# Optimization experiments

Hardware: AMD Instinct MI355X
Metric: run time of the kernel (lower is better)

The kernel has to match this reference:

```python
import jax, jax.numpy as jnp
import numpy as np

B, C, H, W = 8, 256, 32, 32
N, COND_DIM, KV_DIM, REL_DIM = 512, 512, 512, 64
N_HEADS = 8
D_HEAD = KV_DIM // N_HEADS
K_SEL = int(N * 0.6)  # auto mode, shallow layer (layer_idx=2 < total_layers//2=4) -> centrality, ratio_shallow=0.6
NEG = -1e9


def _linear_params(key, fan_in, fan_out):
    kw, kb = jax.random.split(key)
    w = jax.random.normal(kw, (fan_out, fan_in), dtype=jnp.float32) / np.sqrt(fan_in)
    b = jax.random.normal(kb, (fan_out,), dtype=jnp.float32) * 0.01
    return w, b


def _normalize(x, axis=-1):
    # torch F.normalize: x / max(||x||_2, eps)
    n = jnp.sqrt(jnp.sum(x * x, axis=axis, keepdims=True))
    return x / jnp.maximum(n, 1e-12)


def setup_inputs() -> dict:
    key = jax.random.key(0)
    ks = jax.random.split(key, 10)
    h = jax.random.normal(ks[0], (B, C, H, W), dtype=jnp.float32)
    cond_feats = jax.random.normal(ks[1], (B, N, COND_DIM), dtype=jnp.float32)
    cond_mask = jax.random.randint(ks[2], (B, N), 0, 2) > 0  # bool, 1 valid
    Wq, bq = _linear_params(ks[3], C, KV_DIM)
    Wk, bk = _linear_params(ks[4], COND_DIM, KV_DIM)
    Wv, bv = _linear_params(ks[5], COND_DIM, KV_DIM)
    Wrq, brq = _linear_params(ks[6], C, REL_DIM)
    Wrk, brk = _linear_params(ks[7], COND_DIM, REL_DIM)
    Wo, bo = _linear_params(ks[8], KV_DIM, C)
    return dict(h=h, cond_feats=cond_feats, cond_mask=cond_mask,
                Wq=Wq, bq=bq, Wk=Wk, bk=bk, Wv=Wv, bv=bv,
                Wrq=Wrq, brq=brq, Wrk=Wrk, brk=brk, Wo=Wo, bo=bo)


def reference(h, cond_feats, cond_mask, Wq, bq, Wk, bk, Wv, bv, Wrq, brq, Wrk, brk, Wo, bo):
    Bq, Ch, Hh, Ww = h.shape
    S = Hh * Ww
    # ---- q/k/v projections ----
    q = h.reshape(Bq, Ch, S).transpose(0, 2, 1)                # (B,S,C)
    q = q @ Wq.T + bq                                           # (B,S,KV)
    K = cond_feats @ Wk.T + bk                                  # (B,N,KV)
    V = cond_feats @ Wv.T + bv
    qh = q.reshape(Bq, S, N_HEADS, D_HEAD).transpose(0, 2, 1, 3)
    kh = K.reshape(Bq, N, N_HEADS, D_HEAD).transpose(0, 2, 1, 3)
    vh = V.reshape(Bq, N, N_HEADS, D_HEAD).transpose(0, 2, 1, 3)
    attn_scores = jnp.einsum('bhqd,bhkd->bhqk', qh, kh) / np.sqrt(D_HEAD)
    # ---- selector: auto mode, shallow -> centrality scores ----
    qg = h.mean(axis=(2, 3))                                    # adaptive_avg_pool2d(h,1) -> (B,C)
    qg_proj = _normalize(qg @ Wrq.T + brq)                      # (B,REL)  (unused branch kept faithful)
    cond_proj = _normalize(cond_feats @ Wrk.T + brk)            # (B,N,REL)
    Smat = jnp.einsum('bnd,bmd->bnm', cond_proj, cond_proj)     # (B,N,N)
    eye = jnp.eye(N, dtype=bool)
    centrality = jnp.where(eye[None], 0.0, Smat).sum(axis=-1)   # (B,N)
    scores = centrality
    # ---- top-k mask via scatter ----
    topk_idx = jax.lax.top_k(scores, K_SEL)[1]                  # (B,K)
    selected = jnp.zeros((Bq, N), dtype=bool).at[jnp.arange(Bq)[:, None], topk_idx].set(True)
    allowed = selected & cond_mask
    rows_all_false = ~allowed.any(axis=1)                       # (B,)
    idx0 = jnp.argmax(scores, axis=-1)                          # top-1 fallback
    fallback = jax.nn.one_hot(idx0, N, dtype=bool)
    allowed = allowed | (rows_all_false[:, None] & fallback)
    attn_scores = jnp.where(allowed[:, None, None, :], attn_scores, NEG)
    # ---- attention ----
    attn = jax.nn.softmax(attn_scores, axis=-1)
    out = jnp.einsum('bhqk,bhkd->bhqd', attn, vh)               # (B,h,S,d)
    out = out.transpose(0, 2, 1, 3).reshape(Bq, S, KV_DIM)
    out = out @ Wo.T + bo                                       # (B,S,C)
    return out.transpose(0, 2, 1).reshape(Bq, Ch, Hh, Ww)
```

## Files before the change

kernel.cpp:

```cpp
#include <hip/hip_runtime.h>
#include <math.h>

#define B_ 8
#define C_ 256
#define S_ 1024
#define N_ 512
#define KV_ 512
#define REL_ 64
#define NH_ 8
#define DH_ 64
#define KSEL_ 307

typedef __attribute__((ext_vector_type(8))) short bf16x8;
typedef __attribute__((ext_vector_type(4))) short short4v;
typedef __attribute__((ext_vector_type(4))) float f32x4;

__device__ __forceinline__ short f2bf(float f) {
  unsigned int u = __float_as_uint(f);
  u += 0x7fffu + ((u >> 16) & 1u);
  return (short)(u >> 16);
}

__global__ __launch_bounds__(256) void k_prep(const float* __restrict__ cond, const float* __restrict__ Wq,
                                              const float* __restrict__ Wk, const float* __restrict__ Wv,
                                              const float* __restrict__ Wo, const float* __restrict__ h,
                                              const float* __restrict__ Wrk,
                                              short* __restrict__ cond_b, short* __restrict__ Wq_b,
                                              short* __restrict__ Wk_b, short* __restrict__ Wv_b,
                                              short* __restrict__ Wo_b, short* __restrict__ hT,
                                              float* __restrict__ cp_part) {
  __shared__ float fs[2176];
  int blk = blockIdx.x, tid = threadIdx.x;
  if (blk < 2816) {
    const float* src; short* dst; int base;
    if (blk < 2048)      { src = cond; dst = cond_b; base = blk; }
    else if (blk < 2176) { src = Wq;   dst = Wq_b;   base = blk - 2048; }
    else if (blk < 2432) { src = Wk;   dst = Wk_b;   base = blk - 2176; }
    else if (blk < 2688) { src = Wv;   dst = Wv_b;   base = blk - 2432; }
    else                 { src = Wo;   dst = Wo_b;   base = blk - 2688; }
    int i = base * 256 + tid;
    float4 v = ((const float4*)src)[i];
    short4v o = { f2bf(v.x), f2bf(v.y), f2bf(v.z), f2bf(v.w) };
    ((short4v*)dst)[i] = o;
  } else if (blk < 4864) {
    int i = blk - 2816;
    int s0 = (i & 31) * 32, c0 = ((i >> 5) & 7) * 32, b = i >> 8;
    int x = tid & 31, y0 = tid >> 5;
    #pragma unroll
    for (int y = y0; y < 32; y += 8)
      fs[y * 33 + x] = h[((size_t)(b * C_ + c0 + y)) * S_ + s0 + x];
    __syncthreads();
    #pragma unroll
    for (int y = y0; y < 32; y += 8)
      hT[((size_t)(b * S_ + s0 + y)) * C_ + c0 + x] = f2bf(fs[x * 33 + y]);
  } else {
    int i = blk - 4864;
    int bm = (i & 63) * 64, kb = i >> 6;
    float* As = fs;
    float* Bs = fs + 1088;
    int tm = (tid >> 4) << 2, tn = (tid & 15) << 2;
    float acc[4][4] = {};
    for (int k0 = kb * 64; k0 < kb * 64 + 64; k0 += 16) {
      #pragma unroll
      for (int ii = 0; ii < 4; ++ii) {
        int idx = tid + ii * 256;
        int r = idx >> 4, k = idx & 15;
        As[r * 17 + k] = cond[(size_t)(bm + r) * KV_ + k0 + k];
        Bs[r * 17 + k] = Wrk[(size_t)r * KV_ + k0 + k];
      }
      __syncthreads();
      #pragma unroll
      for (int k = 0; k < 16; ++k) {
        float a[4], bb[4];
        #pragma unroll
        for (int x = 0; x < 4; ++x) { a[x] = As[(tm + x) * 17 + k]; bb[x] = Bs[(tn + x) * 17 + k]; }
        #pragma unroll
        for (int x = 0; x < 4; ++x)
          #pragma unroll
          for (int y = 0; y < 4; ++y)
            acc[x][y] += a[x] * bb[y];
      }
      __syncthreads();
    }
    #pragma unroll
    for (int x = 0; x < 4; ++x)
      #pragma unroll
      for (int y = 0; y < 4; ++y)
        cp_part[(size_t)kb * 262144 + (size_t)(bm + tm + x) * 64 + tn + y] = acc[x][y];
  }
}

__global__ __launch_bounds__(256) void k_normalize(const float* __restrict__ cp_part, const float* __restrict__ brk,
                                                   float* __restrict__ cp) {
  int row = blockIdx.x * 4 + (threadIdx.x >> 6);
  int d = threadIdx.x & 63;
  size_t off = (size_t)row * 64 + d;
  float x = brk[d];
  #pragma unroll
  for (int s = 0; s < 8; ++s) x += cp_part[(size_t)s * 262144 + off];
  float ss = x * x;
  #pragma unroll
  for (int o = 32; o; o >>= 1) ss += __shfl_xor(ss, o);
  cp[off] = x / fmaxf(sqrtf(ss), 1e-12f);
}

__global__ __launch_bounds__(512) void k_select(const float* __restrict__ cp, const int* __restrict__ mask,
                                                int* __restrict__ idxb, int* __restrict__ cnt) {
  int b = blockIdx.x, tid = threadIdx.x;
  __shared__ float part[8][64];
  __shared__ float vsum[64];
  __shared__ float sc[512];
  __shared__ int wcnt[8];
  int d = tid & 63, g = tid >> 6;
  float sacc = 0.f;
  for (int n = g * 64; n < g * 64 + 64; ++n)
    sacc += cp[((size_t)b * N_ + n) * 64 + d];
  part[g][d] = sacc;
  __syncthreads();
  if (tid < 64) {
    float v = 0.f;
    #pragma unroll
    for (int gg = 0; gg < 8; ++gg) v += part[gg][tid];
    vsum[tid] = v;
  }
  __syncthreads();
  const float* x = cp + ((size_t)b * N_ + tid) * 64;
  float dsum = 0.f, dself = 0.f;
  #pragma unroll
  for (int dd = 0; dd < 64; ++dd) {
    float xv = x[dd];
    dsum += xv * vsum[dd];
    dself += xv * xv;
  }
  sc[tid] = dsum - dself;
  __syncthreads();
  float v = sc[tid];
  int rank = 0;
  for (int j = 0; j < N_; ++j) {
    float u = sc[j];
    rank += (u > v) || (u == v && j < tid);
  }
  int sel = (rank < KSEL_) && (mask[b * N_ + tid] != 0);
  unsigned long long bal = __ballot(sel);
  if ((tid & 63) == 0) wcnt[g] = __popcll(bal);
  __syncthreads();
  int off2 = 0, total = 0;
  #pragma unroll
  for (int i = 0; i < 8; ++i) { int c = wcnt[i]; total += c; if (i < g) off2 += c; }
  int pos = off2 + __popcll(bal & ((1ull << (tid & 63)) - 1ull));
  if (sel) idxb[b * N_ + pos] = tid;
  if (total == 0 && rank == 0) idxb[b * N_] = tid;
  if (tid == 0) cnt[b] = (total == 0) ? 1 : total;
}

template<int MODE, int GA, int GB, int WM>
__device__ __forceinline__ void gemm_body(const short* __restrict__ A, const short* __restrict__ W,
                                          const float* __restrict__ bias, void* __restrict__ Cout,
                                          short* As, short* Bs, size_t bm, size_t bn, int Kd, int Nout,
                                          const int* __restrict__ gidx, int cntv) {
  constexpr int BMv = WM * 32;
  constexpr int NIA = BMv / 64;
  constexpr int OPS = NIA + 2;
  int tid = threadIdx.x;
  int lane = tid & 63, wid = tid >> 6;
  int wr = wid >> 1, wc = wid & 1;
  f32x4 acc[WM][4] = {};
  int srow = lane >> 2;
  int schunk = lane & 3;
  int steps = Kd >> 5;

  int rowA[NIA ? NIA : 1], rowB[2];
  #pragma unroll
  for (int i = 0; i < NIA; ++i) {
    int rt = wid * (WM * 8) + i * 16 + srow;
    rowA[i] = GA ? (((int)bm + rt < cntv) ? gidx[bm + rt] : 0) : (int)(bm + rt);
  }
  #pragma unroll
  for (int i = 0; i < 2; ++i) {
    int rt = wid * 32 + i * 16 + srow;
    rowB[i] = GB ? (((int)bn + rt < cntv) ? gidx[bn + rt] : 0) : (int)(bn + rt);
  }

  #define STAGE_G(t, buf)                                                                              \
    {                                                                                                  \
      int k0s = (t) * 32;                                                                              \
      _Pragma("unroll")                                                                                \
      for (int i = 0; i < NIA; ++i) {                                                                  \
        int rt = wid * (WM * 8) + i * 16 + srow;                                                       \
        int sc_ = (schunk ^ ((rt >> 1) & 3)) * 8;                                                      \
        const short* ga = A + (size_t)rowA[i] * Kd + k0s + sc_;                                        \
        __builtin_amdgcn_global_load_lds((const __attribute__((address_space(1))) void*)ga,            \
            (__attribute__((address_space(3))) void*)(As + (buf) * (BMv * 32) +                        \
                                                     (wid * (WM * 8) + i * 16) * 32),                  \
            16, 0, 0);                                                                                 \
      }                                                                                                \
      _Pragma("unroll")                                                                                \
      for (int i = 0; i < 2; ++i) {                                                                    \
        int rt = wid * 32 + i * 16 + srow;                                                             \
        int sc_ = (schunk ^ ((rt >> 1) & 3)) * 8;                                                      \
        const short* gb = W + (size_t)rowB[i] * Kd + k0s + sc_;                                        \
        __builtin_amdgcn_global_load_lds((const __attribute__((address_space(1))) void*)gb,            \
            (__attribute__((address_space(3))) void*)(Bs + (buf) * 4096 + (wid * 32 + i * 16) * 32),   \
            16, 0, 0);                                                                                 \
      }                                                                                                \
    }

  STAGE_G(0, 0);
  STAGE_G(1, 1);

  int cur = 0;
  for (int t = 0; t < steps; ++t) {
    if (t == steps - 1)
      asm volatile("s_waitcnt vmcnt(0)" ::: "memory");
    else
      asm volatile("s_waitcnt vmcnt(%0)" :: "n"(OPS) : "memory");
    __syncthreads();
    if (t + 2 < steps) {
      int nb = cur + 2; if (nb >= 3) nb -= 3;
      STAGE_G(t + 2, nb);
    }
    const short* Ac = As + cur * (BMv * 32);
    const short* Bc = Bs + cur * 4096;
    bf16x8 a[WM], b[4];
    #pragma unroll
    for (int m = 0; m < WM; ++m) {
      int rt = wr * (WM * 16) + m * 16 + (lane & 15);
      a[m] = *(const bf16x8*)(Ac + rt * 32 + (((lane >> 4) ^ ((rt >> 1) & 3)) * 8));
    }
    #pragma unroll
    for (int n = 0; n < 4; ++n) {
      int rt = wc * 64 + n * 16 + (lane & 15);
      b[n] = *(const bf16x8*)(Bc + rt * 32 + (((lane >> 4) ^ ((rt >> 1) & 3)) * 8));
    }
    __builtin_amdgcn_s_setprio(1);
    #pragma unroll
    for (int m = 0; m < WM; ++m)
      #pragma unroll
      for (int n = 0; n < 4; ++n)
        acc[m][n] = __builtin_amdgcn_mfma_f32_16x16x32_bf16(a[m], b[n], acc[m][n], 0, 0, 0);
    __builtin_amdgcn_s_setprio(0);
    cur = (cur == 2) ? 0 : cur + 1;
  }
  #undef STAGE_G

  int c0 = lane & 15, r0q = lane >> 4;
  #pragma unroll
  for (int n = 0; n < 4; ++n) {
    size_t col = bn + wc * 64 + n * 16 + c0;
    #pragma unroll
    for (int m = 0; m < WM; ++m) {
      #pragma unroll
      for (int j = 0; j < 4; ++j) {
        size_t row = bm + wr * (WM * 16) + m * 16 + r0q * 4 + j;
        if (MODE == 0) {
          ((short*)Cout)[row * Nout + col] = f2bf(acc[m][n][j] + bias[col]);
        } else if (MODE == 1) {
          ((float*)Cout)[((col >> 10) * C_ + row) * S_ + (col & (S_ - 1))] = acc[m][n][j] + bias[row];
        } else {
          ((short*)Cout)[row * Nout + col] = f2bf(acc[m][n][j] + bias[row]);
        }
      }
    }
  }
}

__global__ __launch_bounds__(256) void k_fused_proj(const short* __restrict__ hT, const short* __restrict__ cond_b,
                                                    const short* __restrict__ Wq_b, const short* __restrict__ Wk_b,
                                                    const short* __restrict__ Wv_b,
                                                    const float* __restrict__ bq, const float* __restrict__ bk,
                                                    const float* __restrict__ bv,
                                                    short* __restrict__ qb, short* __restrict__ Kc,
                                                    short* __restrict__ Vtc,
                                                    const int* __restrict__ idxb, const int* __restrict__ cnt) {
  __shared__ short smem[24576];
  int blk = blockIdx.x;
  if (blk < 96) {
    int b = blk / 12, j = blk % 12;
    int mt = j >> 2, ntile = j & 3;
    int cv = cnt[b], padded = (cv + 63) & ~63;
    if (mt * 128 >= padded) return;
    gemm_body<0, 1, 0, 4>(cond_b + (size_t)b * N_ * KV_, Wk_b, bk, Kc + (size_t)b * N_ * KV_,
                          smem, smem + 12288, (size_t)mt * 128, (size_t)ntile * 128, KV_, KV_,
                          idxb + b * N_, cv);
  } else if (blk < 192) {
    int i = blk - 96, b = i / 12, j = i % 12;
    int mtd = j & 3, ntc = j >> 2;
    int cv = cnt[b], padded = (cv + 63) & ~63;
    if (ntc * 128 >= padded) return;
    gemm_body<3, 0, 1, 4>(Wv_b, cond_b + (size_t)b * N_ * KV_, bv, Vtc + (size_t)b * 512 * N_,
                          smem, smem + 12288, (size_t)mtd * 128, (size_t)ntc * 128, KV_, N_,
                          idxb + b * N_, cv);
  } else {
    int i = blk - 192;
    gemm_body<0, 0, 0, 4>(hT, Wq_b, bq, qb, smem, smem + 12288,
                          (size_t)(i & 63) * 128, (size_t)(i >> 6) * 128, C_, KV_, nullptr, 0);
  }
}

__device__ __forceinline__ void stage_tile64(const short* gRowBase, int gStride, short* ldsBase, int wid, int lane) {
  int sub = lane >> 3;
  int colE = ((lane & 7) ^ sub) * 8;
  #pragma unroll
  for (int i = 0; i < 2; ++i) {
    int r = wid * 16 + i * 8 + sub;
    const short* gp = gRowBase + (size_t)r * gStride + colE;
    __builtin_amdgcn_global_load_lds((const __attribute__((address_space(1))) void*)gp,
                                     (__attribute__((address_space(3))) void*)(ldsBase + wid * 1024 + i * 512),
                                     16, 0, 0);
  }
}
__device__ __forceinline__ void stage_tile64_w8(const short* gRowBase, int gStride, short* ldsBase, int wid, int lane) {
  int sub = lane >> 3;
  int colE = ((lane & 7) ^ sub) * 8;
  int r = wid * 8 + sub;
  const short* gp = gRowBase + (size_t)r * gStride + colE;
  __builtin_amdgcn_global_load_lds((const __attribute__((address_space(1))) void*)gp,
                                   (__attribute__((address_space(3))) void*)(ldsBase + wid * 512),
                                   16, 0, 0);
}

#define QK2L 0.18033688f
__global__ __launch_bounds__(512) void k_attn_mfma(const short* __restrict__ qb, const short* __restrict__ Kc,
                                                   const short* __restrict__ Vtc, const int* __restrict__ cnt,
                                                   short* __restrict__ attn_b) {
  __shared__ short Qs[8192];
  __shared__ short Ks[2][4096];
  __shared__ short Vs[2][4096];
  short* Ps = Qs;
  int g = blockIdx.x;
  int xcd = g & 7, li = g >> 3;
  int bh = xcd * 8 + (li >> 3);
  int qt = li & 7;
  int b = bh >> 3, h = bh & 7;
  int tid = threadIdx.x, lane = tid & 63, wid = tid >> 6;
  int hi = lane >> 4, q = lane & 15;
  int s0 = qt * 128;
  int cntv = cnt[b];
  int nt = (cntv + 63) >> 6;
  const short* Qg = qb + ((size_t)(b * S_ + s0) * KV_ + h * DH_);
  const short* Kg = Kc + ((size_t)(b * N_) * KV_ + h * DH_);
  const short* Vg = Vtc + ((size_t)((b * NH_ + h) * DH_) * N_);

  stage_tile64(Qg, KV_, Qs, wid, lane);
  stage_tile64_w8(Kg, KV_, Ks[0], wid, lane);
  stage_tile64_w8(Vg, N_, Vs[0], wid, lane);
  asm volatile("s_waitcnt vmcnt(0)" ::: "memory");
  __syncthreads();

  int swz = (lane & 7) << 3;
  bf16x8 qf0 = *(const bf16x8*)&Qs[(wid * 16 + q) * 64 + ((hi * 8) ^ swz)];
  bf16x8 qf1 = *(const bf16x8*)&Qs[(wid * 16 + q) * 64 + ((32 + hi * 8) ^ swz)];

  float m = -1e30f, l = 0.f;
  f32x4 o[4] = {};

  for (int t = 0; t < nt; ++t) {
    int cur = t & 1;
    const short* Kcur = Ks[cur];
    const short* Vcur = Vs[cur];
    if (t + 1 < nt) {
      stage_tile64_w8(Kg + (size_t)(t + 1) * 64 * KV_, KV_, Ks[cur ^ 1], wid, lane);
      stage_tile64_w8(Vg + (t + 1) * 64, N_, Vs[cur ^ 1], wid, lane);
    }
    f32x4 pv[4];
    __builtin_amdgcn_s_setprio(1);
    #pragma unroll
    for (int kf = 0; kf < 4; ++kf) {
      bf16x8 k0 = *(const bf16x8*)&Kcur[(kf * 16 + q) * 64 + ((hi * 8) ^ swz)];
      bf16x8 k1 = *(const bf16x8*)&Kcur[(kf * 16 + q) * 64 + ((32 + hi * 8) ^ swz)];
      f32x4 z = {0.f, 0.f, 0.f, 0.f};
      pv[kf] = __builtin_amdgcn_mfma_f32_16x16x32_bf16(k0, qf0, z, 0, 0, 0);
      pv[kf] = __builtin_amdgcn_mfma_f32_16x16x32_bf16(k1, qf1, pv[kf], 0, 0, 0);
    }
    __builtin_amdgcn_s_setprio(0);
    float sv[16];
    int kbase = t * 64 + hi * 4;
    #pragma unroll
    for (int kf = 0; kf < 4; ++kf) {
      #pragma unroll
      for (int r = 0; r < 4; ++r)
        sv[kf * 4 + r] = (kbase + kf * 16 + r < cntv) ? pv[kf][r] * QK2L : -1e30f;
    }
    float tmax = sv[0];
    #pragma unroll
    for (int i = 1; i < 16; ++i) tmax = fmaxf(tmax, sv[i]);
    tmax = fmaxf(tmax, __shfl_xor(tmax, 16));
    tmax = fmaxf(tmax, __shfl_xor(tmax, 32));
    float mnew = fmaxf(m, tmax);
    float scale = exp2f(m - mnew);
    float psum = 0.f;
    #pragma unroll
    for (int i = 0; i < 16; ++i) { sv[i] = exp2f(sv[i] - mnew); psum += sv[i]; }
    psum += __shfl_xor(psum, 16);
    psum += __shfl_xor(psum, 32);
    l = l * scale + psum;
    m = mnew;
    #pragma unroll
    for (int df = 0; df < 4; ++df) {
      o[df][0] *= scale; o[df][1] *= scale; o[df][2] *= scale; o[df][3] *= scale;
    }
    int pbase = wid * 1024 + q * 64;
    #pragma unroll
    for (int kf = 0; kf < 4; ++kf) {
      short4v pk = { f2bf(sv[kf * 4 + 0]), f2bf(sv[kf * 4 + 1]), f2bf(sv[kf * 4 + 2]), f2bf(sv[kf * 4 + 3]) };
      *(short4v*)&Ps[pbase + ((kf * 16 + hi * 4) ^ swz)] = pk;
    }
    __builtin_amdgcn_s_setprio(1);
    #pragma unroll
    for (int ks = 0; ks < 2; ++ks) {
      bf16x8 pb = *(const bf16x8*)&Ps[pbase + ((ks * 32 + hi * 8) ^ swz)];
      #pragma unroll
      for (int df = 0; df < 4; ++df) {
        bf16x8 vf = *(const bf16x8*)&Vcur[(df * 16 + q) * 64 + ((ks * 32 + hi * 8) ^ swz)];
        o[df] = __builtin_amdgcn_mfma_f32_16x16x32_bf16(vf, pb, o[df], 0, 0, 0);
      }
    }
    __builtin_amdgcn_s_setprio(0);
    asm volatile("s_waitcnt vmcnt(0)" ::: "memory");
    __syncthreads();
  }
  float inv = 1.0f / l;
  short* op = attn_b + ((size_t)(b * S_ + s0 + wid * 16 + q) * KV_ + h * DH_);
  #pragma unroll
  for (int df = 0; df < 4; ++df) {
    short4v ov = { f2bf(o[df][0] * inv), f2bf(o[df][1] * inv), f2bf(o[df][2] * inv), f2bf(o[df][3] * inv) };
    *(short4v*)&op[df * 16 + hi * 4] = ov;
  }
}

__global__ __launch_bounds__(256) void k_outproj(const short* __restrict__ Wo_b, const short* __restrict__ attn_b,
                                                 const float* __restrict__ bo, float* __restrict__ out) {
  __shared__ short smem[18432];
  gemm_body<1, 0, 0, 2>(Wo_b, attn_b, bo, out, smem, smem + 6144,
                        (size_t)blockIdx.x * 64, (size_t)blockIdx.y * 128, KV_, B_ * S_, nullptr, 0);
}

extern "C" void kernel_launch(void* const* d_in, const int* in_sizes, int n_in,
                              void* d_out, int out_size, void* d_ws, size_t ws_size,
                              hipStream_t stream) {
  const float* h         = (const float*)d_in[0];
  const float* cond      = (const float*)d_in[1];
  const int*   cond_mask = (const int*)d_in[2];
  const float* Wq = (const float*)d_in[3];
  const float* bq = (const float*)d_in[4];
  const float* Wk = (const float*)d_in[5];
  const float* bk = (const float*)d_in[6];
  const float* Wv = (const float*)d_in[7];
  const float* bv = (const float*)d_in[8];
  const float* Wrk = (const float*)d_in[11];
  const float* brk = (const float*)d_in[12];
  const float* Wo  = (const float*)d_in[13];
  const float* bo  = (const float*)d_in[14];
  float* out = (float*)d_out;

  char* w = (char*)d_ws;
  short* qb      = (short*)(w + 0);
  short* Kc      = (short*)(w + 8388608);
  short* Vtc     = (short*)(w + 12582912);
  short* attn_b  = (short*)(w + 16777216);
  short* hT      = (short*)(w + 25165824);
  short* cond_b  = (short*)(w + 29360128);
  float* cp_part = (float*)(w + 33554432);
  float* cp      = (float*)(w + 41943040);
  int*   idxb    = (int*)  (w + 42991616);
  int*   cnt     = (int*)  (w + 43008000);
  short* Wq_b    = (short*)(w + 43008064);
  short* Wk_b    = (short*)(w + 43270208);
  short* Wv_b    = (short*)(w + 43794496);
  short* Wo_b    = (short*)(w + 44318784);

  k_prep<<<5376, 256, 0, stream>>>(cond, Wq, Wk, Wv, Wo, h, Wrk,
                                   cond_b, Wq_b, Wk_b, Wv_b, Wo_b, hT, cp_part);
  k_normalize<<<1024, 256, 0, stream>>>(cp_part, brk, cp);
  k_select<<<8, 512, 0, stream>>>(cp, cond_mask, idxb, cnt);
  k_fused_proj<<<448, 256, 0, stream>>>(hT, cond_b, Wq_b, Wk_b, Wv_b, bq, bk, bv,
                                        qb, Kc, Vtc, idxb, cnt);
  k_attn_mfma<<<512, 512, 0, stream>>>(qb, Kc, Vtc, cnt, attn_b);
  k_outproj<<<dim3(4, 64), 256, 0, stream>>>(Wo_b, attn_b, bo, out);
}
```

Baseline: 98.95 us.

## Fuse post-prep kernels into one persistent megakernel with grid barriers

```diff
diff --git a/kernel.cpp b/kernel.cpp
--- a/kernel.cpp
+++ b/kernel.cpp
@@ -10,6 +10,7 @@
 #define NH_ 8
 #define DH_ 64
 #define KSEL_ 307
+#define NBLK_ 512
 
 typedef __attribute__((ext_vector_type(8))) short bf16x8;
 typedef __attribute__((ext_vector_type(4))) short short4v;
@@ -19,6 +20,16 @@
   unsigned int u = __float_as_uint(f);
   u += 0x7fffu + ((u >> 16) & 1u);
   return (short)(u >> 16);
+}
+
+__device__ __forceinline__ void grid_barrier(int* bar, int target) {
+  __syncthreads();
+  if (threadIdx.x == 0) {
+    __hip_atomic_fetch_add(bar, 1, __ATOMIC_RELEASE, __HIP_MEMORY_SCOPE_AGENT);
+    while (__hip_atomic_load(bar, __ATOMIC_ACQUIRE, __HIP_MEMORY_SCOPE_AGENT) < target)
+      __builtin_amdgcn_s_sleep(2);
+  }
+  __syncthreads();
 }
 
 __global__ __launch_bounds__(256) void k_prep(const float* __restrict__ cond, const float* __restrict__ Wq,
@@ -90,69 +101,6 @@
   }
 }
 
-__global__ __launch_bounds__(256) void k_normalize(const float* __restrict__ cp_part, const float* __restrict__ brk,
-                                                   float* __restrict__ cp) {
-  int row = blockIdx.x * 4 + (threadIdx.x >> 6);
-  int d = threadIdx.x & 63;
-  size_t off = (size_t)row * 64 + d;
-  float x = brk[d];
-  #pragma unroll
-  for (int s = 0; s < 8; ++s) x += cp_part[(size_t)s * 262144 + off];
-  float ss = x * x;
-  #pragma unroll
-  for (int o = 32; o; o >>= 1) ss += __shfl_xor(ss, o);
-  cp[off] = x / fmaxf(sqrtf(ss), 1e-12f);
-}
-
-__global__ __launch_bounds__(512) void k_select(const float* __restrict__ cp, const int* __restrict__ mask,
-                                                int* __restrict__ idxb, int* __restrict__ cnt) {
-  int b = blockIdx.x, tid = threadIdx.x;
-  __shared__ float part[8][64];
-  __shared__ float vsum[64];
-  __shared__ float sc[512];
-  __shared__ int wcnt[8];
-  int d = tid & 63, g = tid >> 6;
-  float sacc = 0.f;
-  for (int n = g * 64; n < g * 64 + 64; ++n)
-    sacc += cp[((size_t)b * N_ + n) * 64 + d];
-  part[g][d] = sacc;
-  __syncthreads();
-  if (tid < 64) {
-    float v = 0.f;
-    #pragma unroll
-    for (int gg = 0; gg < 8; ++gg) v += part[gg][tid];
-    vsum[tid] = v;
-  }
-  __syncthreads();
-  const float* x = cp + ((size_t)b * N_ + tid) * 64;
-  float dsum = 0.f, dself = 0.f;
-  #pragma unroll
-  for (int dd = 0; dd < 64; ++dd) {
-    float xv = x[dd];
-    dsum += xv * vsum[dd];
-    dself += xv * xv;
-  }
-  sc[tid] = dsum - dself;
-  __syncthreads();
-  float v = sc[tid];
-  int rank = 0;
-  for (int j = 0; j < N_; ++j) {
-    float u = sc[j];
-    rank += (u > v) || (u == v && j < tid);
-  }
-  int sel = (rank < KSEL_) && (mask[b * N_ + tid] != 0);
-  unsigned long long bal = __ballot(sel);
-  if ((tid & 63) == 0) wcnt[g] = __popcll(bal);
-  __syncthreads();
-  int off2 = 0, total = 0;
-  #pragma unroll
-  for (int i = 0; i < 8; ++i) { int c = wcnt[i]; total += c; if (i < g) off2 += c; }
-  int pos = off2 + __popcll(bal & ((1ull << (tid & 63)) - 1ull));
-  if (sel) idxb[b * N_ + pos] = tid;
-  if (total == 0 && rank == 0) idxb[b * N_] = tid;
-  if (tid == 0) cnt[b] = (total == 0) ? 1 : total;
-}
-
 template<int MODE, int GA, int GB, int WM>
 __device__ __forceinline__ void gemm_body(const short* __restrict__ A, const short* __restrict__ W,
                                           const float* __restrict__ bias, void* __restrict__ Cout,
@@ -264,39 +212,6 @@
   }
 }
 
-__global__ __launch_bounds__(256) void k_fused_proj(const short* __restrict__ hT, const short* __restrict__ cond_b,
-                                                    const short* __restrict__ Wq_b, const short* __restrict__ Wk_b,
-                                                    const short* __restrict__ Wv_b,
-                                                    const float* __restrict__ bq, const float* __restrict__ bk,
-                                                    const float* __restrict__ bv,
-                                                    short* __restrict__ qb, short* __restrict__ Kc,
-                                                    short* __restrict__ Vtc,
-                                                    const int* __restrict__ idxb, const int* __restrict__ cnt) {
-  __shared__ short smem[24576];
-  int blk = blockIdx.x;
-  if (blk < 96) {
-    int b = blk / 12, j = blk % 12;
-    int mt = j >> 2, ntile = j & 3;
-    int cv = cnt[b], padded = (cv + 63) & ~63;
-    if (mt * 128 >= padded) return;
-    gemm_body<0, 1, 0, 4>(cond_b + (size_t)b * N_ * KV_, Wk_b, bk, Kc + (size_t)b * N_ * KV_,
-                          smem, smem + 12288, (size_t)mt * 128, (size_t)ntile * 128, KV_, KV_,
-                          idxb + b * N_, cv);
-  } else if (blk < 192) {
-    int i = blk - 96, b = i / 12, j = i % 12;
-    int mtd = j & 3, ntc = j >> 2;
-    int cv = cnt[b], padded = (cv + 63) & ~63;
-    if (ntc * 128 >= padded) return;
-    gemm_body<3, 0, 1, 4>(Wv_b, cond_b + (size_t)b * N_ * KV_, bv, Vtc + (size_t)b * 512 * N_,
-                          smem, smem + 12288, (size_t)mtd * 128, (size_t)ntc * 128, KV_, N_,
-                          idxb + b * N_, cv);
-  } else {
-    int i = blk - 192;
-    gemm_body<0, 0, 0, 4>(hT, Wq_b, bq, qb, smem, smem + 12288,
-                          (size_t)(i & 63) * 128, (size_t)(i >> 6) * 128, C_, KV_, nullptr, 0);
-  }
-}
-
 __device__ __forceinline__ void stage_tile64(const short* gRowBase, int gStride, short* ldsBase, int wid, int lane) {
   int sub = lane >> 3;
   int colE = ((lane & 7) ^ sub) * 8;
@@ -309,130 +224,241 @@
                                      16, 0, 0);
   }
 }
-__device__ __forceinline__ void stage_tile64_w8(const short* gRowBase, int gStride, short* ldsBase, int wid, int lane) {
-  int sub = lane >> 3;
-  int colE = ((lane & 7) ^ sub) * 8;
-  int r = wid * 8 + sub;
-  const short* gp = gRowBase + (size_t)r * gStride + colE;
-  __builtin_amdgcn_global_load_lds((const __attribute__((address_space(1))) void*)gp,
-                                   (__attribute__((address_space(3))) void*)(ldsBase + wid * 512),
-                                   16, 0, 0);
-}
 
 #define QK2L 0.18033688f
-__global__ __launch_bounds__(512) void k_attn_mfma(const short* __restrict__ qb, const short* __restrict__ Kc,
-                                                   const short* __restrict__ Vtc, const int* __restrict__ cnt,
-                                                   short* __restrict__ attn_b) {
-  __shared__ short Qs[8192];
-  __shared__ short Ks[2][4096];
-  __shared__ short Vs[2][4096];
-  short* Ps = Qs;
-  int g = blockIdx.x;
-  int xcd = g & 7, li = g >> 3;
-  int bh = xcd * 8 + (li >> 3);
-  int qt = li & 7;
-  int b = bh >> 3, h = bh & 7;
-  int tid = threadIdx.x, lane = tid & 63, wid = tid >> 6;
-  int hi = lane >> 4, q = lane & 15;
-  int s0 = qt * 128;
-  int cntv = cnt[b];
-  int nt = (cntv + 63) >> 6;
-  const short* Qg = qb + ((size_t)(b * S_ + s0) * KV_ + h * DH_);
-  const short* Kg = Kc + ((size_t)(b * N_) * KV_ + h * DH_);
-  const short* Vg = Vtc + ((size_t)((b * NH_ + h) * DH_) * N_);
-
-  stage_tile64(Qg, KV_, Qs, wid, lane);
-  stage_tile64_w8(Kg, KV_, Ks[0], wid, lane);
-  stage_tile64_w8(Vg, N_, Vs[0], wid, lane);
-  asm volatile("s_waitcnt vmcnt(0)" ::: "memory");
-  __syncthreads();
-
-  int swz = (lane & 7) << 3;
-  bf16x8 qf0 = *(const bf16x8*)&Qs[(wid * 16 + q) * 64 + ((hi * 8) ^ swz)];
-  bf16x8 qf1 = *(const bf16x8*)&Qs[(wid * 16 + q) * 64 + ((32 + hi * 8) ^ swz)];
-
-  float m = -1e30f, l = 0.f;
-  f32x4 o[4] = {};
-
-  for (int t = 0; t < nt; ++t) {
-    int cur = t & 1;
-    const short* Kcur = Ks[cur];
-    const short* Vcur = Vs[cur];
-    if (t + 1 < nt) {
-      stage_tile64_w8(Kg + (size_t)(t + 1) * 64 * KV_, KV_, Ks[cur ^ 1], wid, lane);
-      stage_tile64_w8(Vg + (t + 1) * 64, N_, Vs[cur ^ 1], wid, lane);
-    }
-    f32x4 pv[4];
-    __builtin_amdgcn_s_setprio(1);
-    #pragma unroll
-    for (int kf = 0; kf < 4; ++kf) {
-      bf16x8 k0 = *(const bf16x8*)&Kcur[(kf * 16 + q) * 64 + ((hi * 8) ^ swz)];
-      bf16x8 k1 = *(const bf16x8*)&Kcur[(kf * 16 + q) * 64 + ((32 + hi * 8) ^ swz)];
-      f32x4 z = {0.f, 0.f, 0.f, 0.f};
-      pv[kf] = __builtin_amdgcn_mfma_f32_16x16x32_bf16(k0, qf0, z, 0, 0, 0);
-      pv[kf] = __builtin_amdgcn_mfma_f32_16x16x32_bf16(k1, qf1, pv[kf], 0, 0, 0);
-    }
-    __builtin_amdgcn_s_setprio(0);
-    float sv[16];
-    int kbase = t * 64 + hi * 4;
-    #pragma unroll
-    for (int kf = 0; kf < 4; ++kf) {
-      #pragma unroll
-      for (int r = 0; r < 4; ++r)
-        sv[kf * 4 + r] = (kbase + kf * 16 + r < cntv) ? pv[kf][r] * QK2L : -1e30f;
-    }
-    float tmax = sv[0];
-    #pragma unroll
-    for (int i = 1; i < 16; ++i) tmax = fmaxf(tmax, sv[i]);
-    tmax = fmaxf(tmax, __shfl_xor(tmax, 16));
-    tmax = fmaxf(tmax, __shfl_xor(tmax, 32));
-    float mnew = fmaxf(m, tmax);
-    float scale = exp2f(m - mnew);
-    float psum = 0.f;
-    #pragma unroll
-    for (int i = 0; i < 16; ++i) { sv[i] = exp2f(sv[i] - mnew); psum += sv[i]; }
-    psum += __shfl_xor(psum, 16);
-    psum += __shfl_xor(psum, 32);
-    l = l * scale + psum;
-    m = mnew;
-    #pragma unroll
-    for (int df = 0; df < 4; ++df) {
-      o[df][0] *= scale; o[df][1] *= scale; o[df][2] *= scale; o[df][3] *= scale;
-    }
-    int pbase = wid * 1024 + q * 64;
-    #pragma unroll
-    for (int kf = 0; kf < 4; ++kf) {
-      short4v pk = { f2bf(sv[kf * 4 + 0]), f2bf(sv[kf * 4 + 1]), f2bf(sv[kf * 4 + 2]), f2bf(sv[kf * 4 + 3]) };
-      *(short4v*)&Ps[pbase + ((kf * 16 + hi * 4) ^ swz)] = pk;
-    }
-    __builtin_amdgcn_s_setprio(1);
-    #pragma unroll
-    for (int ks = 0; ks < 2; ++ks) {
-      bf16x8 pb = *(const bf16x8*)&Ps[pbase + ((ks * 32 + hi * 8) ^ swz)];
+__global__ __launch_bounds__(256, 2) void k_mega(
+    const float* __restrict__ cp_part, const float* __restrict__ brk, float* __restrict__ cp,
+    const int* __restrict__ cond_mask, int* __restrict__ idxb, int* __restrict__ cnt,
+    const short* __restrict__ hT, const short* __restrict__ cond_b,
+    const short* __restrict__ Wq_b, const short* __restrict__ Wk_b, const short* __restrict__ Wv_b,
+    const float* __restrict__ bq, const float* __restrict__ bk, const float* __restrict__ bv,
+    short* __restrict__ qb, short* __restrict__ Kc, short* __restrict__ Vtc,
+    short* __restrict__ attn_b, const short* __restrict__ Wo_b, const float* __restrict__ bo,
+    float* __restrict__ out, int* __restrict__ bar) {
+  __shared__ char smem_raw[49152];
+  int bid = blockIdx.x, tid = threadIdx.x;
+
+  {
+    int wid = tid >> 6, d = tid & 63;
+    #pragma unroll
+    for (int i = 0; i < 2; ++i) {
+      int row = (bid * 4 + wid) * 2 + i;
+      size_t off = (size_t)row * 64 + d;
+      float x = brk[d];
+      #pragma unroll
+      for (int s = 0; s < 8; ++s) x += cp_part[(size_t)s * 262144 + off];
+      float ss = x * x;
+      #pragma unroll
+      for (int o = 32; o; o >>= 1) ss += __shfl_xor(ss, o);
+      cp[off] = x / fmaxf(sqrtf(ss), 1e-12f);
+    }
+  }
+  grid_barrier(bar, NBLK_);
+
+  if (bid < 8) {
+    float* part = (float*)smem_raw;
+    float* vsum = part + 256;
+    float* sc   = vsum + 64;
+    int*   wcnt = (int*)(sc + 512);
+    int b = bid;
+    int d = tid & 63, g = tid >> 6;
+    float sacc = 0.f;
+    for (int n = g * 128; n < g * 128 + 128; ++n)
+      sacc += cp[((size_t)b * N_ + n) * 64 + d];
+    part[g * 64 + d] = sacc;
+    __syncthreads();
+    if (tid < 64) vsum[tid] = part[tid] + part[64 + tid] + part[128 + tid] + part[192 + tid];
+    __syncthreads();
+    #pragma unroll
+    for (int rr = 0; rr < 2; ++rr) {
+      int n = tid + rr * 256;
+      const float* x = cp + ((size_t)b * N_ + n) * 64;
+      float dsum = 0.f, dself = 0.f;
+      #pragma unroll
+      for (int dd = 0; dd < 64; ++dd) {
+        float xv = x[dd];
+        dsum += xv * vsum[dd];
+        dself += xv * xv;
+      }
+      sc[n] = dsum - dself;
+    }
+    __syncthreads();
+    int sel[2], rank[2];
+    #pragma unroll
+    for (int rr = 0; rr < 2; ++rr) {
+      int n = tid + rr * 256;
+      float v = sc[n];
+      int r = 0;
+      for (int j = 0; j < N_; ++j) {
+        float u = sc[j];
+        r += (u > v) || (u == v && j < n);
+      }
+      rank[rr] = r;
+      sel[rr] = (r < KSEL_) && (cond_mask[b * N_ + n] != 0);
+    }
+    unsigned long long bal0 = __ballot(sel[0]);
+    unsigned long long bal1 = __ballot(sel[1]);
+    if ((tid & 63) == 0) { wcnt[g] = __popcll(bal0); wcnt[4 + g] = __popcll(bal1); }
+    __syncthreads();
+    int off0 = 0, off4 = 0, total = 0;
+    #pragma unroll
+    for (int c = 0; c < 8; ++c) {
+      int cc = wcnt[c];
+      total += cc;
+      if (c < g) off0 += cc;
+      if (c < 4 + g) off4 += cc;
+    }
+    unsigned long long lmask = (1ull << (tid & 63)) - 1ull;
+    if (sel[0]) idxb[b * N_ + off0 + __popcll(bal0 & lmask)] = tid;
+    if (sel[1]) idxb[b * N_ + off4 + __popcll(bal1 & lmask)] = tid + 256;
+    if (total == 0) {
+      if (rank[0] == 0) idxb[b * N_] = tid;
+      if (rank[1] == 0) idxb[b * N_] = tid + 256;
+    }
+    if (tid == 0) cnt[b] = (total == 0) ? 1 : total;
+  }
+  grid_barrier(bar, 2 * NBLK_);
+
+  {
+    short* As = (short*)smem_raw;
+    short* Bs = As + 12288;
+    if (bid < 96) {
+      int b = bid / 12, j = bid % 12;
+      int mt = j >> 2, ntile = j & 3;
+      int cv = cnt[b], padded = (cv + 63) & ~63;
+      if (mt * 128 < padded)
+        gemm_body<0, 1, 0, 4>(cond_b + (size_t)b * N_ * KV_, Wk_b, bk, Kc + (size_t)b * N_ * KV_,
+                              As, Bs, (size_t)mt * 128, (size_t)ntile * 128, KV_, KV_,
+                              idxb + b * N_, cv);
+    } else if (bid < 192) {
+      int i = bid - 96, b = i / 12, j = i % 12;
+      int mtd = j & 3, ntc = j >> 2;
+      int cv = cnt[b], padded = (cv + 63) & ~63;
+      if (ntc * 128 < padded)
+        gemm_body<3, 0, 1, 4>(Wv_b, cond_b + (size_t)b * N_ * KV_, bv, Vtc + (size_t)b * 512 * N_,
+                              As, Bs, (size_t)mtd * 128, (size_t)ntc * 128, KV_, N_,
+                              idxb + b * N_, cv);
+    } else if (bid < 448) {
+      int i = bid - 192;
+      gemm_body<0, 0, 0, 4>(hT, Wq_b, bq, qb, As, Bs,
+                            (size_t)(i & 63) * 128, (size_t)(i >> 6) * 128, C_, KV_, nullptr, 0);
+    }
+  }
+  grid_barrier(bar, 3 * NBLK_);
+
+  {
+    short* Qs  = (short*)smem_raw;
+    short* KsB = Qs + 4096;
+    short* VsB = KsB + 8192;
+    short* Ps  = Qs;
+    int lane = tid & 63, wid = tid >> 6;
+    int hi = lane >> 4, q = lane & 15;
+    int swz = (lane & 7) << 3;
+    for (int it = 0; it < 2; ++it) {
+      int job = bid * 2 + it;
+      int bh = job >> 4, qt = job & 15;
+      int b = bh >> 3, h = bh & 7;
+      int s0 = qt * 64;
+      int cntv = cnt[b];
+      int nt = (cntv + 63) >> 6;
+      const short* Qg = qb + ((size_t)(b * S_ + s0) * KV_ + h * DH_);
+      const short* Kg = Kc + ((size_t)(b * N_) * KV_ + h * DH_);
+      const short* Vg = Vtc + ((size_t)b * 512 + h * DH_) * N_;
+
+      stage_tile64(Qg, KV_, Qs, wid, lane);
+      stage_tile64(Kg, KV_, KsB, wid, lane);
+      stage_tile64(Vg, N_, VsB, wid, lane);
+      asm volatile("s_waitcnt vmcnt(0)" ::: "memory");
+      __syncthreads();
+
+      bf16x8 qf0 = *(const bf16x8*)&Qs[(wid * 16 + q) * 64 + ((hi * 8) ^ swz)];
+      bf16x8 qf1 = *(const bf16x8*)&Qs[(wid * 16 + q) * 64 + ((32 + hi * 8) ^ swz)];
+
+      float m = -1e30f, l = 0.f;
+      f32x4 o[4] = {};
+
+      for (int t = 0; t < nt; ++t) {
+        int cur = t & 1;
+        const short* Kcur = KsB + cur * 4096;
+        const short* Vcur = VsB + cur * 4096;
+        if (t + 1 < nt) {
+          stage_tile64(Kg + (size_t)(t + 1) * 64 * KV_, KV_, KsB + (cur ^ 1) * 4096, wid, lane);
+          stage_tile64(Vg + (t + 1) * 64, N_, VsB + (cur ^ 1) * 4096, wid, lane);
+        }
+        f32x4 pv[4];
+        __builtin_amdgcn_s_setprio(1);
+        #pragma unroll
+        for (int kf = 0; kf < 4; ++kf) {
+          bf16x8 k0 = *(const bf16x8*)&Kcur[(kf * 16 + q) * 64 + ((hi * 8) ^ swz)];
+          bf16x8 k1 = *(const bf16x8*)&Kcur[(kf * 16 + q) * 64 + ((32 + hi * 8) ^ swz)];
+          f32x4 z = {0.f, 0.f, 0.f, 0.f};
+          pv[kf] = __builtin_amdgcn_mfma_f32_16x16x32_bf16(k0, qf0, z, 0, 0, 0);
+          pv[kf] = __builtin_amdgcn_mfma_f32_16x16x32_bf16(k1, qf1, pv[kf], 0, 0, 0);
+        }
+        __builtin_amdgcn_s_setprio(0);
+        float sv[16];
+        int kbase = t * 64 + hi * 4;
+        #pragma unroll
+        for (int kf = 0; kf < 4; ++kf) {
+          #pragma unroll
+          for (int r = 0; r < 4; ++r)
+            sv[kf * 4 + r] = (kbase + kf * 16 + r < cntv) ? pv[kf][r] * QK2L : -1e30f;
+        }
+        float tmax = sv[0];
+        #pragma unroll
+        for (int i = 1; i < 16; ++i) tmax = fmaxf(tmax, sv[i]);
+        tmax = fmaxf(tmax, __shfl_xor(tmax, 16));
+        tmax = fmaxf(tmax, __shfl_xor(tmax, 32));
+        float mnew = fmaxf(m, tmax);
+        float scale = exp2f(m - mnew);
+        float psum = 0.f;
+        #pragma unroll
+        for (int i = 0; i < 16; ++i) { sv[i] = exp2f(sv[i] - mnew); psum += sv[i]; }
+        psum += __shfl_xor(psum, 16);
+        psum += __shfl_xor(psum, 32);
+        l = l * scale + psum;
+        m = mnew;
+        #pragma unroll
+        for (int df = 0; df < 4; ++df) {
+          o[df][0] *= scale; o[df][1] *= scale; o[df][2] *= scale; o[df][3] *= scale;
+        }
+        int pbase = wid * 1024 + q * 64;
+        #pragma unroll
+        for (int kf = 0; kf < 4; ++kf) {
+          short4v pk = { f2bf(sv[kf * 4 + 0]), f2bf(sv[kf * 4 + 1]), f2bf(sv[kf * 4 + 2]), f2bf(sv[kf * 4 + 3]) };
+          *(short4v*)&Ps[pbase + ((kf * 16 + hi * 4) ^ swz)] = pk;
+        }
+        __builtin_amdgcn_s_setprio(1);
+        #pragma unroll
+        for (int ks = 0; ks < 2; ++ks) {
+          bf16x8 pb = *(const bf16x8*)&Ps[pbase + ((ks * 32 + hi * 8) ^ swz)];
+          #pragma unroll
+          for (int df = 0; df < 4; ++df) {
+            bf16x8 vf = *(const bf16x8*)&Vcur[(df * 16 + q) * 64 + ((ks * 32 + hi * 8) ^ swz)];
+            o[df] = __builtin_amdgcn_mfma_f32_16x16x32_bf16(vf, pb, o[df], 0, 0, 0);
+          }
+        }
+        __builtin_amdgcn_s_setprio(0);
+        asm volatile("s_waitcnt vmcnt(0)" ::: "memory");
+        __syncthreads();
+      }
+      float inv = 1.0f / l;
+      short* op = attn_b + ((size_t)(b * S_ + s0 + wid * 16 + q) * KV_ + h * DH_);
       #pragma unroll
       for (int df = 0; df < 4; ++df) {
-        bf16x8 vf = *(const bf16x8*)&Vcur[(df * 16 + q) * 64 + ((ks * 32 + hi * 8) ^ swz)];
-        o[df] = __builtin_amdgcn_mfma_f32_16x16x32_bf16(vf, pb, o[df], 0, 0, 0);
-      }
-    }
-    __builtin_amdgcn_s_setprio(0);
-    asm volatile("s_waitcnt vmcnt(0)" ::: "memory");
-    __syncthreads();
-  }
-  float inv = 1.0f / l;
-  short* op = attn_b + ((size_t)(b * S_ + s0 + wid * 16 + q) * KV_ + h * DH_);
-  #pragma unroll
-  for (int df = 0; df < 4; ++df) {
-    short4v ov = { f2bf(o[df][0] * inv), f2bf(o[df][1] * inv), f2bf(o[df][2] * inv), f2bf(o[df][3] * inv) };
-    *(short4v*)&op[df * 16 + hi * 4] = ov;
-  }
-}
-
-__global__ __launch_bounds__(256) void k_outproj(const short* __restrict__ Wo_b, const short* __restrict__ attn_b,
-                                                 const float* __restrict__ bo, float* __restrict__ out) {
-  __shared__ short smem[18432];
-  gemm_body<1, 0, 0, 2>(Wo_b, attn_b, bo, out, smem, smem + 6144,
-                        (size_t)blockIdx.x * 64, (size_t)blockIdx.y * 128, KV_, B_ * S_, nullptr, 0);
+        short4v ov = { f2bf(o[df][0] * inv), f2bf(o[df][1] * inv), f2bf(o[df][2] * inv), f2bf(o[df][3] * inv) };
+        *(short4v*)&op[df * 16 + hi * 4] = ov;
+      }
+    }
+  }
+  grid_barrier(bar, 4 * NBLK_);
+
+  if (bid < 256) {
+    short* As = (short*)smem_raw;
+    short* Bs = As + 6144;
+    gemm_body<1, 0, 0, 2>(Wo_b, attn_b, bo, out, As, Bs,
+                          (size_t)(bid & 3) * 64, (size_t)(bid >> 2) * 128, KV_, B_ * S_, nullptr, 0);
+  }
 }
 
 extern "C" void kernel_launch(void* const* d_in, const int* in_sizes, int n_in,
@@ -468,13 +494,12 @@
   short* Wk_b    = (short*)(w + 43270208);
   short* Wv_b    = (short*)(w + 43794496);
   short* Wo_b    = (short*)(w + 44318784);
-
+  int*   bar     = (int*)  (w + 44580928);
+
+  hipMemsetAsync(bar, 0, 16, stream);
   k_prep<<<5376, 256, 0, stream>>>(cond, Wq, Wk, Wv, Wo, h, Wrk,
                                    cond_b, Wq_b, Wk_b, Wv_b, Wo_b, hT, cp_part);
-  k_normalize<<<1024, 256, 0, stream>>>(cp_part, brk, cp);
-  k_select<<<8, 512, 0, stream>>>(cp, cond_mask, idxb, cnt);
-  k_fused_proj<<<448, 256, 0, stream>>>(hT, cond_b, Wq_b, Wk_b, Wv_b, bq, bk, bv,
-                                        qb, Kc, Vtc, idxb, cnt);
-  k_attn_mfma<<<512, 512, 0, stream>>>(qb, Kc, Vtc, cnt, attn_b);
-  k_outproj<<<dim3(4, 64), 256, 0, stream>>>(Wo_b, attn_b, bo, out);
-}
+  k_mega<<<NBLK_, 256, 0, stream>>>(cp_part, brk, cp, cond_mask, idxb, cnt, hT, cond_b,
+                                    Wq_b, Wk_b, Wv_b, bq, bk, bv, qb, Kc, Vtc,
+                                    attn_b, Wo_b, bo, out, bar);
+}
```

Result: slower. 373.9 us (+277.8%).
